# Optimization experiments

Measured on AMD Instinct MI355X. Metric: run time of the kernel, lower is better.

The kernel has to match this reference:

```python
import jax, jax.numpy as jnp
import numpy as np

B, C, H = 8, 512, 2048
GROUPS = 32
EPS = 1e-6


def setup_inputs() -> dict:
    key = jax.random.key(0)
    ks = jax.random.split(key, 10)
    s = 1.0 / np.sqrt(C)
    return {
        "x": jax.random.normal(ks[0], (B, C, H), dtype=jnp.float32),
        "gamma": jnp.ones((C,), jnp.float32),
        "beta": jnp.zeros((C,), jnp.float32),
        "wq": jax.random.normal(ks[1], (C, C), jnp.float32) * s,
        "bq": jnp.zeros((C,), jnp.float32),
        "wk": jax.random.normal(ks[2], (C, C), jnp.float32) * s,
        "bk": jnp.zeros((C,), jnp.float32),
        "wv": jax.random.normal(ks[3], (C, C), jnp.float32) * s,
        "bv": jnp.zeros((C,), jnp.float32),
        "wp": jax.random.normal(ks[4], (C, C), jnp.float32) * s,
        "bp": jnp.zeros((C,), jnp.float32),
    }


def group_norm(x, gamma, beta):
    b, c, h = x.shape
    xr = x.reshape(b, GROUPS, c // GROUPS, h)
    mean = xr.mean(axis=(2, 3), keepdims=True)
    var = xr.var(axis=(2, 3), keepdims=True)
    xn = ((xr - mean) * jax.lax.rsqrt(var + EPS)).reshape(b, c, h)
    return xn * gamma[None, :, None] + beta[None, :, None]


def conv1x1(x, w, b):
    # 1x1 Conv1d == channel-mixing GEMM: [C_out,C_in] x [b,C_in,h]
    return jnp.einsum("oc,bch->boh", w, x) + b[None, :, None]


def reference(x, gamma, beta, wq, bq, wk, bk, wv, bv, wp, bp):
    b, c, h = x.shape
    hn = group_norm(x, gamma, beta)
    q = conv1x1(hn, wq, bq)  # [b,c,h]
    k = conv1x1(hn, wk, bk)
    v = conv1x1(hn, wv, bv)
    # scores w[b,i,j] = sum_c q[b,c,i] k[b,c,j] / sqrt(c)
    w = jnp.einsum("bci,bcj->bij", q, k) * (c ** -0.5)
    w = jax.nn.softmax(w, axis=2)
    # h_[b,c,i] = sum_j v[b,c,j] w[b,i,j]
    h_ = jnp.einsum("bcj,bij->bci", v, w)
    out = conv1x1(h_, wp, bp)
    return x + out
```

## Files before the change

### kernel.cpp

```cpp
#include <hip/hip_runtime.h>
#include <stdint.h>

typedef unsigned short u16;
typedef short s16x8 __attribute__((ext_vector_type(8)));
typedef float f32x4 __attribute__((ext_vector_type(4)));

#define BM 128
#define BN 128
#define BK 32
#define KPAD 40

__device__ __forceinline__ float bf2f(u16 b) {
    union { unsigned int u; float f; } v; v.u = ((unsigned int)b) << 16; return v.f;
}
__device__ __forceinline__ u16 f2bf(float f) {
    union { float f; unsigned int u; } v; v.f = f;
    unsigned int u = v.u;
    u += 0x7fffu + ((u >> 16) & 1u);
    return (u16)(u >> 16);
}
__device__ __forceinline__ void async_cp16(const u16* g, u16* l) {
    __builtin_amdgcn_global_load_lds((const __attribute__((address_space(1))) void*)g,
                                     (__attribute__((address_space(3))) void*)l, 16, 0, 0);
}

__global__ __launch_bounds__(256) void gn_stats(const float* __restrict__ x,
                                                float* __restrict__ mean,
                                                float* __restrict__ rstd) {
    const int bg = blockIdx.x;
    const float* p = x + (long)bg * 16 * 2048;
    float s = 0.f, ss = 0.f;
    for (int it = 0; it < 32; it++) {
        const float4 v = *reinterpret_cast<const float4*>(p + ((it * 256 + threadIdx.x) << 2));
        s += v.x + v.y + v.z + v.w;
        ss += v.x * v.x + v.y * v.y + v.z * v.z + v.w * v.w;
    }
    const int lane = threadIdx.x & 63, wave = threadIdx.x >> 6;
#pragma unroll
    for (int o = 32; o > 0; o >>= 1) { s += __shfl_down(s, o, 64); ss += __shfl_down(ss, o, 64); }
    __shared__ float rb[8];
    if (lane == 0) { rb[wave] = s; rb[4 + wave] = ss; }
    __syncthreads();
    if (threadIdx.x == 0) {
        float S = rb[0] + rb[1] + rb[2] + rb[3];
        float SS = rb[4] + rb[5] + rb[6] + rb[7];
        float mu = S * (1.f / 32768.f);
        float var = SS * (1.f / 32768.f) - mu * mu;
        mean[bg] = mu;
        rstd[bg] = rsqrtf(var + 1e-6f);
    }
}

__global__ __launch_bounds__(256) void gn_apply_t(const float* __restrict__ x,
                                                  const float* __restrict__ gamma,
                                                  const float* __restrict__ beta,
                                                  const float* __restrict__ mean,
                                                  const float* __restrict__ rstd,
                                                  u16* __restrict__ hnT) {
    const int b = blockIdx.z, c0 = blockIdx.y * 64, h0 = blockIdx.x * 64;
    __shared__ __align__(16) u16 T[64][72];
    const int tid = threadIdx.x;
#pragma unroll
    for (int sidx = 0; sidx < 4; sidx++) {
        int ch = tid + sidx * 256;
        int cc = ch >> 4, h4 = (ch & 15) * 4;
        int c = c0 + cc;
        float mu = mean[b * 32 + (c >> 4)], rs = rstd[b * 32 + (c >> 4)];
        float ga = gamma[c], be = beta[c];
        const float4 v = *reinterpret_cast<const float4*>(x + ((long)b * 512 + c) * 2048 + h0 + h4);
        ushort4 pk;
        pk.x = f2bf((v.x - mu) * rs * ga + be);
        pk.y = f2bf((v.y - mu) * rs * ga + be);
        pk.z = f2bf((v.z - mu) * rs * ga + be);
        pk.w = f2bf((v.w - mu) * rs * ga + be);
        *reinterpret_cast<ushort4*>(&T[cc][h4]) = pk;
    }
    __syncthreads();
#pragma unroll
    for (int sidx = 0; sidx < 2; sidx++) {
        int ch = tid + sidx * 256;
        int hh = ch >> 3, c8 = (ch & 7) * 8;
        unsigned int o[4];
#pragma unroll
        for (int i = 0; i < 4; i++) {
            u16 lo = T[c8 + 2 * i][hh];
            u16 hi = T[c8 + 2 * i + 1][hh];
            o[i] = (unsigned int)lo | ((unsigned int)hi << 16);
        }
        *reinterpret_cast<uint4*>(hnT + ((long)b * 2048 + h0 + hh) * 512 + c0 + c8) =
            uint4{o[0], o[1], o[2], o[3]};
    }
}

__global__ __launch_bounds__(256) void w2bf(const float* __restrict__ a,
                                            const float* __restrict__ b,
                                            const float* __restrict__ c,
                                            u16* __restrict__ dst) {
    const float* s = (blockIdx.y == 0) ? a : (blockIdx.y == 1) ? b : c;
    const int i = (blockIdx.x * 256 + threadIdx.x) * 4;
    const float4 v = *reinterpret_cast<const float4*>(s + i);
    ushort4 p;
    p.x = f2bf(v.x); p.y = f2bf(v.y); p.z = f2bf(v.z); p.w = f2bf(v.w);
    *reinterpret_cast<ushort4*>(dst + (long)blockIdx.y * 262144 + i) = p;
}

__global__ __launch_bounds__(256) void softmax_rows(u16* __restrict__ S) {
    u16* p = S + (long)blockIdx.x * 2048;
    const int tid = threadIdx.x;
    uint4 v = *reinterpret_cast<const uint4*>(p + (tid << 3));
    unsigned int w[4] = {v.x, v.y, v.z, v.w};
    float f[8];
#pragma unroll
    for (int i = 0; i < 4; i++) {
        f[2 * i]     = bf2f((u16)(w[i] & 0xffffu));
        f[2 * i + 1] = bf2f((u16)(w[i] >> 16));
    }
    float m = f[0];
#pragma unroll
    for (int i = 1; i < 8; i++) m = fmaxf(m, f[i]);
    const int lane = tid & 63, wave = tid >> 6;
#pragma unroll
    for (int o = 32; o > 0; o >>= 1) m = fmaxf(m, __shfl_down(m, o, 64));
    __shared__ float rb[4];
    __shared__ float bc;
    if (lane == 0) rb[wave] = m;
    __syncthreads();
    if (tid == 0) bc = fmaxf(fmaxf(rb[0], rb[1]), fmaxf(rb[2], rb[3]));
    __syncthreads();
    m = bc;
    float s = 0.f;
#pragma unroll
    for (int i = 0; i < 8; i++) { f[i] = __expf(f[i] - m); s += f[i]; }
#pragma unroll
    for (int o = 32; o > 0; o >>= 1) s += __shfl_down(s, o, 64);
    __syncthreads();
    if (lane == 0) rb[wave] = s;
    __syncthreads();
    if (tid == 0) bc = 1.f / (rb[0] + rb[1] + rb[2] + rb[3]);
    __syncthreads();
    const float inv = bc;
#pragma unroll
    for (int i = 0; i < 4; i++)
        w[i] = (unsigned int)f2bf(f[2 * i] * inv) | ((unsigned int)f2bf(f[2 * i + 1] * inv) << 16);
    *reinterpret_cast<uint4*>(p + (tid << 3)) = uint4{w[0], w[1], w[2], w[3]};
}

template <int EPI, int SWIZ>
__global__ __launch_bounds__(256) void gemm_tn_a(const u16* __restrict__ Ag, long sA,
                                                 const u16* __restrict__ Bg, long sB,
                                                 const float* __restrict__ bias,
                                                 const float* __restrict__ Xg, long sX,
                                                 void* __restrict__ Ogv, long sO,
                                                 int K, int lda, int ldb, int ldo,
                                                 float scale) {
    const int b = blockIdx.z;
    Ag += (long)b * sA;
    Bg += (long)b * sB;
    int tx, ty;
    if (SWIZ == 1) {
        const int xcd = blockIdx.x & 7, s = blockIdx.x >> 3;
        ty = xcd + 8 * (s >> 2);
        tx = s & 3;
    } else if (SWIZ == 2) {
        const int xcd = blockIdx.x & 7, s = blockIdx.x >> 3;
        ty = (xcd & 3) * 4 + (s & 3);
        tx = (xcd >> 2) * 8 + (s >> 2);
    } else {
        tx = blockIdx.x; ty = blockIdx.y;
    }
    const int m0 = ty * BM;
    const int n0 = tx * BN;

    __shared__ __align__(16) u16 As[2][BM * BK];
    __shared__ __align__(16) u16 Bs[2][BN * BK];

    const int tid = threadIdx.x;
    const int wave = tid >> 6;
    const int lane = tid & 63;
    const int quad = lane >> 4;
    const int l16 = lane & 15;
    const int wm = (wave >> 1) * 64;
    const int wn = (wave & 1) * 64;
    const int rl = lane >> 2;
    const int cl = (lane & 3) * 8;

    f32x4 acc[4][4];
#pragma unroll
    for (int i = 0; i < 4; i++)
#pragma unroll
        for (int j = 0; j < 4; j++) acc[i][j] = f32x4{0.f, 0.f, 0.f, 0.f};

    auto stage = [&](int buf, int k0) {
#pragma unroll
        for (int j = 0; j < 2; j++) {
            const int rbase = wave * 32 + j * 16;
            async_cp16(Ag + (long)(m0 + rbase + rl) * lda + k0 + cl, &As[buf][rbase * BK]);
            async_cp16(Bg + (long)(n0 + rbase + rl) * ldb + k0 + cl, &Bs[buf][rbase * BK]);
        }
    };
    auto compute = [&](int buf) {
        s16x8 af[4], bfr[4];
#pragma unroll
        for (int i = 0; i < 4; i++)
            af[i] = *reinterpret_cast<const s16x8*>(&As[buf][(wm + i * 16 + l16) * BK + quad * 8]);
#pragma unroll
        for (int j = 0; j < 4; j++)
            bfr[j] = *reinterpret_cast<const s16x8*>(&Bs[buf][(wn + j * 16 + l16) * BK + quad * 8]);
#pragma unroll
        for (int i = 0; i < 4; i++)
#pragma unroll
            for (int j = 0; j < 4; j++)
                acc[i][j] = __builtin_amdgcn_mfma_f32_16x16x32_bf16(af[i], bfr[j], acc[i][j], 0, 0, 0);
    };

    stage(0, 0);
    for (int k0 = 0; k0 < K; k0 += 2 * BK) {
        __syncthreads();
        stage(1, k0 + BK);
        compute(0);
        __syncthreads();
        if (k0 + 2 * BK < K) stage(0, k0 + 2 * BK);
        compute(1);
    }

#pragma unroll
    for (int i = 0; i < 4; i++) {
        const int mb = m0 + wm + i * 16 + quad * 4;
#pragma unroll
        for (int j = 0; j < 4; j++) {
            const int n = n0 + wn + j * 16 + l16;
            if (EPI == 0) {
                u16* O = (u16*)Ogv + (long)b * sO;
#pragma unroll
                for (int r = 0; r < 4; r++) {
                    float vv = acc[i][j][r] * scale;
                    if (bias) vv += bias[mb + r];
                    O[(long)(mb + r) * ldo + n] = f2bf(vv);
                }
            } else if (EPI == 1) {
                u16* O = (u16*)Ogv + (long)b * sO;
                ushort4 pk;
                pk.x = f2bf(acc[i][j][0] + bias[mb + 0]);
                pk.y = f2bf(acc[i][j][1] + bias[mb + 1]);
                pk.z = f2bf(acc[i][j][2] + bias[mb + 2]);
                pk.w = f2bf(acc[i][j][3] + bias[mb + 3]);
                *reinterpret_cast<ushort4*>(&O[(long)n * ldo + mb]) = pk;
            } else {
                float* O = (float*)Ogv + (long)b * sO;
                const float* X = Xg + (long)b * sX;
                const float bn = bias[n];
                const float4 xv = *reinterpret_cast<const float4*>(&X[(long)n * ldo + mb]);
                float4 pk;
                pk.x = acc[i][j][0] + bn + xv.x;
                pk.y = acc[i][j][1] + bn + xv.y;
                pk.z = acc[i][j][2] + bn + xv.z;
                pk.w = acc[i][j][3] + bn + xv.w;
                *reinterpret_cast<float4*>(&O[(long)n * ldo + mb]) = pk;
            }
        }
    }
}

__global__ __launch_bounds__(256) void qkv_a(const u16* __restrict__ wb3,
                                             const u16* __restrict__ hnT,
                                             const float* __restrict__ bq,
                                             const float* __restrict__ bk,
                                             const float* __restrict__ bv,
                                             u16* __restrict__ qT, u16* __restrict__ kT,
                                             u16* __restrict__ vv) {
    const long HC = 1048576;
    const int b = blockIdx.z;
    const int xcd = blockIdx.x & 7, s = blockIdx.x >> 3;
    const int hi = (s >= 12) ? 1 : 0;
    const int yy = s - hi * 12;
    const int x = xcd + 8 * hi;
    const int which = yy >> 2;
    const int my = yy & 3;
    const u16* Ag = wb3 + which * 262144;
    const u16* Bg = hnT + (long)b * HC;
    const int m0 = my * BM;
    const int n0 = x * BN;

    __shared__ __align__(16) u16 As[2][BM * BK];
    __shared__ __align__(16) u16 Bs[2][BN * BK];

    const int tid = threadIdx.x;
    const int wave = tid >> 6;
    const int lane = tid & 63;
    const int quad = lane >> 4;
    const int l16 = lane & 15;
    const int wm = (wave >> 1) * 64;
    const int wn = (wave & 1) * 64;
    const int rl = lane >> 2;
    const int cl = (lane & 3) * 8;

    f32x4 acc[4][4];
#pragma unroll
    for (int i = 0; i < 4; i++)
#pragma unroll
        for (int j = 0; j < 4; j++) acc[i][j] = f32x4{0.f, 0.f, 0.f, 0.f};

    auto stage = [&](int buf, int k0) {
#pragma unroll
        for (int j = 0; j < 2; j++) {
            const int rbase = wave * 32 + j * 16;
            async_cp16(Ag + (long)(m0 + rbase + rl) * 512 + k0 + cl, &As[buf][rbase * BK]);
            async_cp16(Bg + (long)(n0 + rbase + rl) * 512 + k0 + cl, &Bs[buf][rbase * BK]);
        }
    };
    auto compute = [&](int buf) {
        s16x8 af[4], bfr[4];
#pragma unroll
        for (int i = 0; i < 4; i++)
            af[i] = *reinterpret_cast<const s16x8*>(&As[buf][(wm + i * 16 + l16) * BK + quad * 8]);
#pragma unroll
        for (int j = 0; j < 4; j++)
            bfr[j] = *reinterpret_cast<const s16x8*>(&Bs[buf][(wn + j * 16 + l16) * BK + quad * 8]);
#pragma unroll
        for (int i = 0; i < 4; i++)
#pragma unroll
            for (int j = 0; j < 4; j++)
                acc[i][j] = __builtin_amdgcn_mfma_f32_16x16x32_bf16(af[i], bfr[j], acc[i][j], 0, 0, 0);
    };

    stage(0, 0);
    for (int k0 = 0; k0 < 512; k0 += 2 * BK) {
        __syncthreads();
        stage(1, k0 + BK);
        compute(0);
        __syncthreads();
        if (k0 + 2 * BK < 512) stage(0, k0 + 2 * BK);
        compute(1);
    }

    if (which == 2) {
        u16* O = vv + (long)b * HC;
#pragma unroll
        for (int i = 0; i < 4; i++) {
            const int mb = m0 + wm + i * 16 + quad * 4;
#pragma unroll
            for (int j = 0; j < 4; j++) {
                const int n = n0 + wn + j * 16 + l16;
#pragma unroll
                for (int r = 0; r < 4; r++)
                    O[(long)(mb + r) * 2048 + n] = f2bf(acc[i][j][r] + bv[mb + r]);
            }
        }
    } else {
        const float* bias = which ? bk : bq;
        u16* O = (which ? kT : qT) + (long)b * HC;
#pragma unroll
        for (int i = 0; i < 4; i++) {
            const int mb = m0 + wm + i * 16 + quad * 4;
#pragma unroll
            for (int j = 0; j < 4; j++) {
                const int n = n0 + wn + j * 16 + l16;
                ushort4 pk;
                pk.x = f2bf(acc[i][j][0] + bias[mb + 0]);
                pk.y = f2bf(acc[i][j][1] + bias[mb + 1]);
                pk.z = f2bf(acc[i][j][2] + bias[mb + 2]);
                pk.w = f2bf(acc[i][j][3] + bias[mb + 3]);
                *reinterpret_cast<ushort4*>(&O[(long)n * 512 + mb]) = pk;
            }
        }
    }
}

template <int F32>
__device__ __forceinline__ void stage_tile(const char* G, int ld, int r0, int k0,
                                           u16* __restrict__ lds, int tid) {
    if (F32) {
        const float* g = (const float*)G;
#pragma unroll
        for (int s = 0; s < 4; s++) {
            const int c = tid + s * 256;
            const int row = c >> 3, col = (c & 7) * 4;
            const float4 v = *reinterpret_cast<const float4*>(g + (long)(r0 + row) * ld + k0 + col);
            ushort4 pk;
            pk.x = f2bf(v.x); pk.y = f2bf(v.y); pk.z = f2bf(v.z); pk.w = f2bf(v.w);
            *reinterpret_cast<ushort4*>(&lds[row * KPAD + col]) = pk;
        }
    } else {
        const u16* g = (const u16*)G;
#pragma unroll
        for (int s = 0; s < 2; s++) {
            const int c = tid + s * 256;
            const int row = c >> 2, col = (c & 3) * 8;
            const uint4 v = *reinterpret_cast<const uint4*>(g + (long)(r0 + row) * ld + k0 + col);
            *reinterpret_cast<uint4*>(&lds[row * KPAD + col]) = v;
        }
    }
}

template <int EPI, int AF32, int BF32>
__global__ __launch_bounds__(256) void gemm_tn(const void* __restrict__ Agv, long sA,
                                               const void* __restrict__ Bgv, long sB,
                                               const float* __restrict__ bias,
                                               const float* __restrict__ Xg, long sX,
                                               void* __restrict__ Ogv, long sO,
                                               int K, int lda, int ldb, int ldo,
                                               float scale) {
    const int b = blockIdx.z;
    const char* A8 = (const char*)Agv + (long)b * sA * (AF32 ? 4 : 2);
    const char* B8 = (const char*)Bgv + (long)b * sB * (BF32 ? 4 : 2);
    const int m0 = blockIdx.y * BM;
    const int n0 = blockIdx.x * BN;

    __shared__ __align__(16) u16 As[BM * KPAD];
    __shared__ __align__(16) u16 Bs[BN * KPAD];

    const int tid = threadIdx.x;
    const int wave = tid >> 6;
    const int lane = tid & 63;
    const int quad = lane >> 4;
    const int l16 = lane & 15;
    const int wm = (wave >> 1) * 64;
    const int wn = (wave & 1) * 64;

    f32x4 acc[4][4];
#pragma unroll
    for (int i = 0; i < 4; i++)
#pragma unroll
        for (int j = 0; j < 4; j++) acc[i][j] = f32x4{0.f, 0.f, 0.f, 0.f};

    for (int k0 = 0; k0 < K; k0 += BK) {
        __syncthreads();
        stage_tile<AF32>(A8, lda, m0, k0, As, tid);
        stage_tile<BF32>(B8, ldb, n0, k0, Bs, tid);
        __syncthreads();
        s16x8 af[4], bfr[4];
#pragma unroll
        for (int i = 0; i < 4; i++)
            af[i] = *reinterpret_cast<const s16x8*>(&As[(wm + i * 16 + l16) * KPAD + quad * 8]);
#pragma unroll
        for (int j = 0; j < 4; j++)
            bfr[j] = *reinterpret_cast<const s16x8*>(&Bs[(wn + j * 16 + l16) * KPAD + quad * 8]);
#pragma unroll
        for (int i = 0; i < 4; i++)
#pragma unroll
            for (int j = 0; j < 4; j++)
                acc[i][j] = __builtin_amdgcn_mfma_f32_16x16x32_bf16(af[i], bfr[j], acc[i][j], 0, 0, 0);
    }

#pragma unroll
    for (int i = 0; i < 4; i++) {
        const int mb = m0 + wm + i * 16 + quad * 4;
#pragma unroll
        for (int j = 0; j < 4; j++) {
            const int n = n0 + wn + j * 16 + l16;
            if (EPI == 0) {
                u16* O = (u16*)Ogv + (long)b * sO;
#pragma unroll
                for (int r = 0; r < 4; r++) {
                    float vv = acc[i][j][r] * scale;
                    if (bias) vv += bias[mb + r];
                    O[(long)(mb + r) * ldo + n] = f2bf(vv);
                }
            } else if (EPI == 1) {
                u16* O = (u16*)Ogv + (long)b * sO;
                ushort4 pk;
                pk.x = f2bf(acc[i][j][0] + bias[mb + 0]);
                pk.y = f2bf(acc[i][j][1] + bias[mb + 1]);
                pk.z = f2bf(acc[i][j][2] + bias[mb + 2]);
                pk.w = f2bf(acc[i][j][3] + bias[mb + 3]);
                *reinterpret_cast<ushort4*>(&O[(long)n * ldo + mb]) = pk;
            } else {
                float* O = (float*)Ogv + (long)b * sO;
                const float* X = Xg + (long)b * sX;
                const float bn = bias[n];
                const float4 xv = *reinterpret_cast<const float4*>(&X[(long)n * ldo + mb]);
                float4 pk;
                pk.x = acc[i][j][0] + bn + xv.x;
                pk.y = acc[i][j][1] + bn + xv.y;
                pk.z = acc[i][j][2] + bn + xv.z;
                pk.w = acc[i][j][3] + bn + xv.w;
                *reinterpret_cast<float4*>(&O[(long)n * ldo + mb]) = pk;
            }
        }
    }
}

extern "C" void kernel_launch(void* const* d_in, const int* in_sizes, int n_in,
                              void* d_out, int out_size, void* d_ws, size_t ws_size,
                              hipStream_t stream) {
    const float* x     = (const float*)d_in[0];
    const float* gamma = (const float*)d_in[1];
    const float* beta  = (const float*)d_in[2];
    const float* wq    = (const float*)d_in[3];
    const float* bq    = (const float*)d_in[4];
    const float* wk    = (const float*)d_in[5];
    const float* bk    = (const float*)d_in[6];
    const float* wv    = (const float*)d_in[7];
    const float* bv    = (const float*)d_in[8];
    const float* wp    = (const float*)d_in[9];
    const float* bp    = (const float*)d_in[10];
    float* out = (float*)d_out;

    const long HC = (long)2048 * 512;
    const long HH = (long)2048 * 2048;
    const long WSZ = 512 * 512;
    const float scl = 0.044194173824159216f;

    char* ws = (char*)d_ws;
    float* meanb = (float*)ws;
    float* rstdb = (float*)(ws + 1024);
    u16* base = (u16*)(ws + 4096);

    const size_t FULL_NEED   = 4096 + 2 * (size_t)(24 * HC + 8 * HH);
    const size_t MED_NEED    = 4096 + 2 * (size_t)(32 * HC + HH);
    const size_t SMALL_NEED  = 4096 + 2 * (size_t)(4 * HC + HH);
    const size_t CHUNK512    = 4096 + 2 * (size_t)(4 * HC + 512 * 2048);

    gn_stats<<<256, 256, 0, stream>>>(x, meanb, rstdb);

    if (ws_size >= FULL_NEED) {
        u16* qT  = base;
        u16* kT  = qT + 8 * HC;
        u16* vv  = kT + 8 * HC;
        u16* Sb  = vv + 8 * HC;
        u16* hnT = Sb;
        u16* wb3 = Sb + 8 * HH - 3 * WSZ;
        u16* hT  = qT;
        u16* wpb = vv;

        w2bf<<<dim3(256, 3), 256, 0, stream>>>(wq, wk, wv, wb3);
        gn_apply_t<<<dim3(32, 8, 8), 256, 0, stream>>>(x, gamma, beta, meanb, rstdb, hnT);
        qkv_a<<<dim3(192, 1, 8), 256, 0, stream>>>(wb3, hnT, bq, bk, bv, qT, kT, vv);
        gemm_tn_a<0, 2><<<dim3(256, 1, 8), 256, 0, stream>>>(qT, HC, kT, HC, nullptr, nullptr, 0,
                                                             Sb, HH, 512, 512, 512, 2048, scl);
        softmax_rows<<<16384, 256, 0, stream>>>(Sb);
        gemm_tn_a<0, 1><<<dim3(64, 1, 8), 256, 0, stream>>>(Sb, HH, vv, HC, nullptr, nullptr, 0,
                                                            hT, HC, 2048, 2048, 2048, 512, 1.f);
        w2bf<<<dim3(256, 1), 256, 0, stream>>>(wp, wp, wp, wpb);
        gemm_tn_a<2, 1><<<dim3(64, 1, 8), 256, 0, stream>>>(hT, HC, wpb, 0, bp, x, HC,
                                                            out, HC, 512, 512, 512, 2048, 1.f);
    } else if (ws_size >= MED_NEED) {
        u16* hnT = base;
        u16* qT  = hnT + 8 * HC;
        u16* kT  = qT + 8 * HC;
        u16* vv  = kT + 8 * HC;
        u16* Sb  = vv + 8 * HC;
        u16* hT  = hnT;
        gn_apply_t<<<dim3(32, 8, 8), 256, 0, stream>>>(x, gamma, beta, meanb, rstdb, hnT);
        gemm_tn<1, 1, 0><<<dim3(16, 4, 8), 256, 0, stream>>>(wq, 0, hnT, HC, bq, nullptr, 0,
                                                             qT, HC, 512, 512, 512, 512, 1.f);
        gemm_tn<1, 1, 0><<<dim3(16, 4, 8), 256, 0, stream>>>(wk, 0, hnT, HC, bk, nullptr, 0,
                                                             kT, HC, 512, 512, 512, 512, 1.f);
        gemm_tn<0, 1, 0><<<dim3(16, 4, 8), 256, 0, stream>>>(wv, 0, hnT, HC, bv, nullptr, 0,
                                                             vv, HC, 512, 512, 512, 2048, 1.f);
        for (int b = 0; b < 8; b++) {
            gemm_tn<0, 0, 0><<<dim3(16, 16, 1), 256, 0, stream>>>(qT + b * HC, 0, kT + b * HC, 0,
                                                                  nullptr, nullptr, 0, Sb, 0,
                                                                  512, 512, 512, 2048, scl);
            softmax_rows<<<2048, 256, 0, stream>>>(Sb);
            gemm_tn<0, 0, 0><<<dim3(4, 16, 1), 256, 0, stream>>>(Sb, 0, vv + b * HC, 0,
                                                                 nullptr, nullptr, 0, hT + b * HC, 0,
                                                                 2048, 2048, 2048, 512, 1.f);
        }
        gemm_tn<2, 0, 1><<<dim3(4, 16, 8), 256, 0, stream>>>(hT, HC, wp, 0, bp, x, HC,
                                                             out, HC, 512, 512, 512, 2048, 1.f);
    } else {
        const int CH = (ws_size >= SMALL_NEED) ? 2048 : ((ws_size >= CHUNK512) ? 512 : 128);
        u16* hn = base;
        u16* q  = hn + HC;
        u16* k  = q + HC;
        u16* v  = k + HC;
        u16* Sc = v + HC;
        u16* hT = hn;
        for (int b = 0; b < 8; b++) {
            const float* xb = x + (long)b * HC;
            gn_apply_t<<<dim3(32, 8, 1), 256, 0, stream>>>(xb, gamma, beta,
                                                           meanb + b * 32, rstdb + b * 32, hn);
            gemm_tn<1, 1, 0><<<dim3(16, 4, 1), 256, 0, stream>>>(wq, 0, hn, 0, bq, nullptr, 0,
                                                                 q, 0, 512, 512, 512, 512, 1.f);
            gemm_tn<1, 1, 0><<<dim3(16, 4, 1), 256, 0, stream>>>(wk, 0, hn, 0, bk, nullptr, 0,
                                                                 k, 0, 512, 512, 512, 512, 1.f);
            gemm_tn<0, 1, 0><<<dim3(16, 4, 1), 256, 0, stream>>>(wv, 0, hn, 0, bv, nullptr, 0,
                                                                 v, 0, 512, 512, 512, 2048, 1.f);
            for (int i0 = 0; i0 < 2048; i0 += CH) {
                gemm_tn<0, 0, 0><<<dim3(16, CH / 128, 1), 256, 0, stream>>>(
                    q + (long)i0 * 512, 0, k, 0, nullptr, nullptr, 0, Sc, 0,
                    512, 512, 512, 2048, scl);
                softmax_rows<<<CH, 256, 0, stream>>>(Sc);
                gemm_tn<0, 0, 0><<<dim3(4, CH / 128, 1), 256, 0, stream>>>(
                    Sc, 0, v, 0, nullptr, nullptr, 0, hT + (long)i0 * 512, 0,
                    2048, 2048, 2048, 512, 1.f);
            }
            gemm_tn<2, 0, 1><<<dim3(4, 16, 1), 256, 0, stream>>>(hT, 0, wp, 0, bp, xb, 0,
                                                                 out + (long)b * HC, 0,
                                                                 512, 512, 512, 2048, 1.f);
        }
    }
}
```

Measured before the change: 317.4 us.

## Triple-buffer LDS in conv GEMM kernels with one barrier per k-step

Both bf16 GEMM kernels (the generic conv1x1 GEMM and the fused QKV projection) move from double-buffered LDS with two __syncthreads per pair of k-steps to a three-stage ring. Each step issues a partial vmcnt wait plus one s_barrier, so two async global-to-LDS stages stay in flight while the current tile feeds the MFMAs. The goal is to hide global load latency and cut barrier overhead. The cost is 50% more LDS per block, which may lower occupancy, and hand-written waitcnt that relies on each stage issuing exactly four loads per thread.

```diff
diff --git a/kernel.cpp b/kernel.cpp
--- a/kernel.cpp
+++ b/kernel.cpp
@@ -171,8 +171,8 @@
     const int m0 = ty * BM;
     const int n0 = tx * BN;
 
-    __shared__ __align__(16) u16 As[2][BM * BK];
-    __shared__ __align__(16) u16 Bs[2][BN * BK];
+    __shared__ __align__(16) u16 As[3][BM * BK];
+    __shared__ __align__(16) u16 Bs[3][BN * BK];
 
     const int tid = threadIdx.x;
     const int wave = tid >> 6;
@@ -213,15 +213,19 @@
                 acc[i][j] = __builtin_amdgcn_mfma_f32_16x16x32_bf16(af[i], bfr[j], acc[i][j], 0, 0, 0);
     };
 
+    const int nsteps = K / BK;
     stage(0, 0);
-    for (int k0 = 0; k0 < K; k0 += 2 * BK) {
-        __syncthreads();
-        stage(1, k0 + BK);
-        compute(0);
-        __syncthreads();
-        if (k0 + 2 * BK < K) stage(0, k0 + 2 * BK);
-        compute(1);
-    }
+    stage(1, BK);
+    int t = 0;
+    for (; t < nsteps - 1; t++) {
+        asm volatile("s_waitcnt vmcnt(4)" ::: "memory");
+        asm volatile("s_barrier" ::: "memory");
+        if (t + 2 < nsteps) stage((t + 2) % 3, (t + 2) * BK);
+        compute(t % 3);
+    }
+    asm volatile("s_waitcnt vmcnt(0)" ::: "memory");
+    asm volatile("s_barrier" ::: "memory");
+    compute(t % 3);
 
 #pragma unroll
     for (int i = 0; i < 4; i++) {
@@ -281,8 +285,8 @@
     const int m0 = my * BM;
     const int n0 = x * BN;
 
-    __shared__ __align__(16) u16 As[2][BM * BK];
-    __shared__ __align__(16) u16 Bs[2][BN * BK];
+    __shared__ __align__(16) u16 As[3][BM * BK];
+    __shared__ __align__(16) u16 Bs[3][BN * BK];
 
     const int tid = threadIdx.x;
     const int wave = tid >> 6;
@@ -323,15 +327,19 @@
                 acc[i][j] = __builtin_amdgcn_mfma_f32_16x16x32_bf16(af[i], bfr[j], acc[i][j], 0, 0, 0);
     };
 
+    const int nsteps = 512 / BK;
     stage(0, 0);
-    for (int k0 = 0; k0 < 512; k0 += 2 * BK) {
-        __syncthreads();
-        stage(1, k0 + BK);
-        compute(0);
-        __syncthreads();
-        if (k0 + 2 * BK < 512) stage(0, k0 + 2 * BK);
-        compute(1);
-    }
+    stage(1, BK);
+    int t = 0;
+    for (; t < nsteps - 1; t++) {
+        asm volatile("s_waitcnt vmcnt(4)" ::: "memory");
+        asm volatile("s_barrier" ::: "memory");
+        if (t + 2 < nsteps) stage((t + 2) % 3, (t + 2) * BK);
+        compute(t % 3);
+    }
+    asm volatile("s_waitcnt vmcnt(0)" ::: "memory");
+    asm volatile("s_barrier" ::: "memory");
+    compute(t % 3);
 
     if (which == 2) {
         u16* O = vv + (long)b * HC;
```

New measurement: 305.9 us. -3.6%, faster.
